# Performance work log

Hardware: AMD Instinct MI355X
Metric: run time of the kernel (lower is better)

The kernel has to match this reference:

```python
import jax, jax.numpy as jnp
import numpy as np

IN_FEATURES = 4096
OUT_FEATURES = 4096
TOKENS = 8192
QMAX = 127.0


def setup_inputs() -> dict:
    key = jax.random.key(0)
    k1, k2, k3, k4 = jax.random.split(key, 4)
    x = jax.random.normal(k1, (TOKENS, IN_FEATURES), dtype=jnp.float32)
    # int8 quantized weights in [-127, 127]
    Wq = jax.random.randint(k2, (OUT_FEATURES, IN_FEATURES), -127, 128, dtype=jnp.int32).astype(jnp.int8)
    # per-row absmax scales (positive)
    row_scales = jax.random.uniform(k3, (OUT_FEATURES,), dtype=jnp.float32, minval=0.01, maxval=1.0)
    bias_param = jax.random.normal(k4, (OUT_FEATURES,), dtype=jnp.float32)
    return {"x": x, "Wq": Wq, "row_scales": row_scales, "bias_param": bias_param}


def reference(x, Wq, row_scales, bias_param):
    # rowwise dequant: W[o, i] = Wq[o, i] * row_scales[o] / 127
    W_dequant = Wq.astype(x.dtype) * (row_scales.astype(x.dtype) / QMAX)[:, None]  # [O, I]
    Y = jnp.matmul(x, W_dequant.T)  # [T, O]
    return Y + bias_param.astype(x.dtype)
```

## Files before the change

### kernel.cpp

```cpp
#include <hip/hip_runtime.h>

#define M_TOK 8192
#define N_OUT 4096
#define K_IN  4096

#define AS1 __attribute__((address_space(1)))
#define AS3 __attribute__((address_space(3)))

typedef __attribute__((ext_vector_type(4))) int i32x4;
typedef __attribute__((ext_vector_type(16))) int i32x16;

template <int OFF>
__device__ __forceinline__ i32x4 dsri(unsigned addr) {
    i32x4 r;
    asm volatile("ds_read_b128 %0, %1 offset:%2" : "=v"(r) : "v"(addr), "n"(OFF));
    return r;
}


__global__ __launch_bounds__(256) void quant_x_kernel(
    const float* __restrict__ x, signed char* __restrict__ xq,
    float* __restrict__ tok_scale)
{
    const int row = blockIdx.x;
    const float4* xr = reinterpret_cast<const float4*>(x + (size_t)row * K_IN);
    const int t = threadIdx.x;
    float4 v[4];
    float m = 0.f;
#pragma unroll
    for (int i = 0; i < 4; ++i) {
        v[i] = xr[t + 256 * i];
        m = fmaxf(m, fmaxf(fmaxf(fabsf(v[i].x), fabsf(v[i].y)),
                           fmaxf(fabsf(v[i].z), fabsf(v[i].w))));
    }
#pragma unroll
    for (int off = 32; off >= 1; off >>= 1)
        m = fmaxf(m, __shfl_xor(m, off, 64));
    __shared__ float wmax[4];
    if ((t & 63) == 0) wmax[t >> 6] = m;
    __syncthreads();
    m = fmaxf(fmaxf(wmax[0], wmax[1]), fmaxf(wmax[2], wmax[3]));
    if (t == 0) tok_scale[row] = m * (1.0f / 127.0f);
    const float inv = (m > 0.f) ? (127.0f / m) : 0.f;
    int* xqi = reinterpret_cast<int*>(xq + (size_t)row * K_IN);
#pragma unroll
    for (int i = 0; i < 4; ++i) {
        const int q0 = __float2int_rn(v[i].x * inv) & 255;
        const int q1 = __float2int_rn(v[i].y * inv) & 255;
        const int q2 = __float2int_rn(v[i].z * inv) & 255;
        const int q3 = __float2int_rn(v[i].w * inv) & 255;
        xqi[t + 256 * i] = q0 | (q1 << 8) | (q2 << 16) | (q3 << 24);
    }
}


__global__ void pack_w_kernel(const int* __restrict__ wq, signed char* __restrict__ o) {
    const int n4 = (N_OUT * K_IN) / 4;
    int* o4 = reinterpret_cast<int*>(o);
    const int stride = gridDim.x * blockDim.x;
    for (int i = blockIdx.x * blockDim.x + threadIdx.x; i < n4; i += stride) {
        const int4 a = reinterpret_cast<const int4*>(wq)[i];
        o4[i] = (a.x & 255) | ((a.y & 255) << 8) | ((a.z & 255) << 16) | ((a.w & 255) << 24);
    }
}


#define BKB 64
#define NKT (K_IN / BKB)
#define SLOT 32768
#define NSLOT 4

#define MFMA(a, b, c) c = __builtin_amdgcn_mfma_i32_32x32x32_i8(a, b, c, 0, 0, 0)

#define RD12(P, aB, bB)                        \
    P##_A0 = dsri<0>(aB);                      \
    P##_A1 = dsri<2048>(aB);                   \
    P##_A2 = dsri<4096>(aB);                   \
    P##_A3 = dsri<6144>(aB);                   \
    P##_B0 = dsri<0>(bB);                      \
    P##_B1 = dsri<2048>(bB);                   \
    P##_A4 = dsri<1024>(aB);                   \
    P##_A5 = dsri<3072>(aB);                   \
    P##_A6 = dsri<5120>(aB);                   \
    P##_A7 = dsri<7168>(aB);                   \
    P##_B2 = dsri<1024>(bB);                   \
    P##_B3 = dsri<3072>(bB);

#define CL8_0(P)                                              \
    MFMA(P##_A0, P##_B0, acc00); MFMA(P##_A0, P##_B1, acc01); \
    MFMA(P##_A1, P##_B0, acc10); MFMA(P##_A1, P##_B1, acc11); \
    MFMA(P##_A2, P##_B0, acc20); MFMA(P##_A2, P##_B1, acc21); \
    MFMA(P##_A3, P##_B0, acc30); MFMA(P##_A3, P##_B1, acc31);

#define CL8_1(P)                                              \
    MFMA(P##_A4, P##_B2, acc00); MFMA(P##_A4, P##_B3, acc01); \
    MFMA(P##_A5, P##_B2, acc10); MFMA(P##_A5, P##_B3, acc11); \
    MFMA(P##_A6, P##_B2, acc20); MFMA(P##_A6, P##_B3, acc21); \
    MFMA(P##_A7, P##_B2, acc30); MFMA(P##_A7, P##_B3, acc31);

#define GBODY(T, C, N, DO_STAGE)                                          \
    {                                                                     \
        asm volatile("s_waitcnt lgkmcnt(6)" ::: "memory");                \
        __builtin_amdgcn_sched_barrier(0);                                \
        __builtin_amdgcn_s_setprio(1);                                    \
        CL8_0(C)                                                          \
        __builtin_amdgcn_s_setprio(0);                                    \
        __builtin_amdgcn_sched_barrier(0);                                \
        const unsigned aN_ = aBase + (unsigned)((((T) + 1) & 3) * SLOT);  \
        const unsigned bN_ = bBase + (unsigned)((((T) + 1) & 3) * SLOT);  \
        RD12(N, aN_, bN_)                                                 \
        if (DO_STAGE) stageAB((T) + 3);                                   \
        asm volatile("s_waitcnt lgkmcnt(12)" ::: "memory");               \
        __builtin_amdgcn_sched_barrier(0);                                \
        __builtin_amdgcn_s_setprio(1);                                    \
        CL8_1(C)                                                          \
        __builtin_amdgcn_s_setprio(0);                                    \
        __builtin_amdgcn_sched_barrier(0);                                \
        if (DO_STAGE) { asm volatile("s_waitcnt vmcnt(4)" ::: "memory"); }\
        else          { asm volatile("s_waitcnt vmcnt(0)" ::: "memory"); }\
        __builtin_amdgcn_sched_barrier(0);                                \
        __builtin_amdgcn_s_barrier();                                     \
        __builtin_amdgcn_sched_barrier(0);                                \
    }

#define GFINAL(C)                                                         \
    {                                                                     \
        asm volatile("s_waitcnt lgkmcnt(6)" ::: "memory");                \
        __builtin_amdgcn_sched_barrier(0);                                \
        __builtin_amdgcn_s_setprio(1);                                    \
        CL8_0(C)                                                          \
        __builtin_amdgcn_s_setprio(0);                                    \
        asm volatile("s_waitcnt lgkmcnt(0)" ::: "memory");                \
        __builtin_amdgcn_sched_barrier(0);                                \
        __builtin_amdgcn_s_setprio(1);                                    \
        CL8_1(C)                                                          \
        __builtin_amdgcn_s_setprio(0);                                    \
        __builtin_amdgcn_sched_barrier(0);                                \
    }

__global__ __launch_bounds__(512, 2) void qgemm_i8p_kernel(
    const signed char* __restrict__ xq,
    const signed char* __restrict__ wq8,
    const float* __restrict__ tok_scale,
    const float* __restrict__ row_scales,
    const float* __restrict__ bias,
    float* __restrict__ out)
{
    __shared__ __align__(16) char smem[NSLOT * SLOT + 1024];

    const int tid = threadIdx.x;
    const int l = tid & 63;
    const int w = tid >> 6;
    const int wr = w >> 2;
    const int wc = w & 3;

    const int bid = blockIdx.x;
    const int swz = (bid & 7) * 64 + (bid >> 3);
    const int bm = swz >> 4;
    const int bn = swz & 15;

    const signed char* aS = xq  + (size_t)(bm * 256 + w * 32 + (l & 31)) * K_IN + (l >> 5) * 16;
    const signed char* bS = wq8 + (size_t)(bn * 256 + w * 32 + (l & 31)) * K_IN + (l >> 5) * 16;
    char* aDst = smem + w * 2048;
    char* bDst = smem + 16384 + w * 2048;

    auto stageAB = [&](int tt) {
        const int sb = (tt & 3) * SLOT;
        const signed char* a0 = aS + tt * BKB;
        const signed char* b0 = bS + tt * BKB;
        __builtin_amdgcn_global_load_lds((const AS1 void*)a0,        (AS3 void*)(aDst + sb),        16, 0, 0);
        __builtin_amdgcn_global_load_lds((const AS1 void*)(a0 + 32), (AS3 void*)(aDst + sb + 1024), 16, 0, 0);
        __builtin_amdgcn_global_load_lds((const AS1 void*)b0,        (AS3 void*)(bDst + sb),        16, 0, 0);
        __builtin_amdgcn_global_load_lds((const AS1 void*)(b0 + 32), (AS3 void*)(bDst + sb + 1024), 16, 0, 0);
    };

    const unsigned sbase = (unsigned)(uintptr_t)(AS3 char*)smem;
    const unsigned aBase = sbase + (unsigned)(wr * 8192 + l * 16);
    const unsigned bBase = sbase + 16384u + (unsigned)(wc * 4096 + l * 16);

    i32x16 acc00 = {0}, acc01 = {0}, acc10 = {0}, acc11 = {0};
    i32x16 acc20 = {0}, acc21 = {0}, acc30 = {0}, acc31 = {0};

    i32x4 X_A0, X_A1, X_A2, X_A3, X_A4, X_A5, X_A6, X_A7, X_B0, X_B1, X_B2, X_B3;
    i32x4 Y_A0, Y_A1, Y_A2, Y_A3, Y_A4, Y_A5, Y_A6, Y_A7, Y_B0, Y_B1, Y_B2, Y_B3;

    stageAB(0); stageAB(1); stageAB(2);
    asm volatile("s_waitcnt vmcnt(4)" ::: "memory");
    __builtin_amdgcn_sched_barrier(0);
    __builtin_amdgcn_s_barrier();
    __builtin_amdgcn_sched_barrier(0);
    RD12(X, aBase, bBase)

    for (int t = 0; t < 62; t += 2) {
        GBODY(t,     X, Y, (t + 3 < NKT));
        GBODY(t + 1, Y, X, (t + 4 < NKT));
    }
    GBODY(62, X, Y, false);
    GFINAL(Y)

    float* ts = (float*)(smem + NSLOT * SLOT);
    if (tid < 256) ts[tid] = tok_scale[bm * 256 + tid];
    __syncthreads();

    const int cl = l & 31;
    const int rg4 = (l >> 5) * 4;
    const int gcol0 = bn * 256 + wc * 64;
    float cs[2], bb[2];
#pragma unroll
    for (int nb = 0; nb < 2; ++nb) {
        const int col = gcol0 + nb * 32 + cl;
        cs[nb] = row_scales[col] * (1.0f / 127.0f);
        bb[nb] = bias[col];
    }
    const i32x16* accs[4][2] = {{&acc00, &acc01}, {&acc10, &acc11},
                                {&acc20, &acc21}, {&acc30, &acc31}};
#pragma unroll
    for (int mb = 0; mb < 4; ++mb) {
#pragma unroll
        for (int reg = 0; reg < 16; ++reg) {
            const int rloc = wr * 128 + mb * 32 + (reg & 3) + 8 * (reg >> 2) + rg4;
            const float tsv = ts[rloc];
            float* orow = out + (size_t)(bm * 256 + rloc) * N_OUT + gcol0 + cl;
#pragma unroll
            for (int nb = 0; nb < 2; ++nb) {
                const int a = (*accs[mb][nb])[reg];
                orow[nb * 32] = (float)a * tsv * cs[nb] + bb[nb];
            }
        }
    }
}


extern "C" void kernel_launch(void* const* d_in, const int* in_sizes, int n_in,
                              void* d_out, int out_size, void* d_ws, size_t ws_size,
                              hipStream_t stream) {
    const float* x = (const float*)d_in[0];
    const int* wq = (const int*)d_in[1];
    const float* row_scales = (const float*)d_in[2];
    const float* bias = (const float*)d_in[3];
    float* out = (float*)d_out;

    signed char* xq8 = (signed char*)d_ws;
    signed char* wq8 = xq8 + (size_t)M_TOK * K_IN;
    float* tok_scale = (float*)(wq8 + (size_t)N_OUT * K_IN);
    (void)ws_size;

    quant_x_kernel<<<M_TOK, 256, 0, stream>>>(x, xq8, tok_scale);
    pack_w_kernel<<<2048, 256, 0, stream>>>(wq, wq8);

    const int nblocks = (M_TOK / 256) * (N_OUT / 256);
    qgemm_i8p_kernel<<<nblocks, 512, 0, stream>>>(
        xq8, wq8, tok_scale, row_scales, bias, out);
}
```

Baseline: 210.5 us.

## Store quantized operands in MFMA fragment-major layout for contiguous GEMM loads

```diff
diff --git a/kernel.cpp b/kernel.cpp
--- a/kernel.cpp
+++ b/kernel.cpp
@@ -17,50 +17,87 @@
     return r;
 }
 
-
-__global__ __launch_bounds__(256) void quant_x_kernel(
-    const float* __restrict__ x, signed char* __restrict__ xq,
+__device__ __forceinline__ int pack4(float a, float b, float c, float d, float inv) {
+    const int q0 = __float2int_rn(a * inv) & 255;
+    const int q1 = __float2int_rn(b * inv) & 255;
+    const int q2 = __float2int_rn(c * inv) & 255;
+    const int q3 = __float2int_rn(d * inv) & 255;
+    return q0 | (q1 << 8) | (q2 << 16) | (q3 << 24);
+}
+
+
+__global__ __launch_bounds__(256) void quant_x_frag_kernel(
+    const float* __restrict__ x, signed char* __restrict__ xqF,
     float* __restrict__ tok_scale)
 {
-    const int row = blockIdx.x;
-    const float4* xr = reinterpret_cast<const float4*>(x + (size_t)row * K_IN);
+    __shared__ float sm_inv[32];
     const int t = threadIdx.x;
-    float4 v[4];
-    float m = 0.f;
-#pragma unroll
-    for (int i = 0; i < 4; ++i) {
-        v[i] = xr[t + 256 * i];
-        m = fmaxf(m, fmaxf(fmaxf(fabsf(v[i].x), fabsf(v[i].y)),
-                           fmaxf(fabsf(v[i].z), fabsf(v[i].w))));
-    }
-#pragma unroll
-    for (int off = 32; off >= 1; off >>= 1)
-        m = fmaxf(m, __shfl_xor(m, off, 64));
-    __shared__ float wmax[4];
-    if ((t & 63) == 0) wmax[t >> 6] = m;
+    const int R0 = blockIdx.x * 32;
+
+    {
+        const int r = R0 + (t >> 3);
+        const float4* xr4 = reinterpret_cast<const float4*>(x) + (size_t)r * 1024;
+        float m = 0.f;
+        for (int p = 0; p < 128; ++p) {
+            const float4 v = xr4[(t & 7) + 8 * p];
+            m = fmaxf(m, fmaxf(fmaxf(fabsf(v.x), fabsf(v.y)),
+                               fmaxf(fabsf(v.z), fabsf(v.w))));
+        }
+        m = fmaxf(m, __shfl_xor(m, 1, 64));
+        m = fmaxf(m, __shfl_xor(m, 2, 64));
+        m = fmaxf(m, __shfl_xor(m, 4, 64));
+        if ((t & 7) == 0) {
+            sm_inv[t >> 3] = (m > 0.f) ? (127.0f / m) : 0.f;
+            tok_scale[r] = m * (1.0f / 127.0f);
+        }
+    }
     __syncthreads();
-    m = fmaxf(fmaxf(wmax[0], wmax[1]), fmaxf(wmax[2], wmax[3]));
-    if (t == 0) tok_scale[row] = m * (1.0f / 127.0f);
-    const float inv = (m > 0.f) ? (127.0f / m) : 0.f;
-    int* xqi = reinterpret_cast<int*>(xq + (size_t)row * K_IN);
-#pragma unroll
-    for (int i = 0; i < 4; ++i) {
-        const int q0 = __float2int_rn(v[i].x * inv) & 255;
-        const int q1 = __float2int_rn(v[i].y * inv) & 255;
-        const int q2 = __float2int_rn(v[i].z * inv) & 255;
-        const int q3 = __float2int_rn(v[i].w * inv) & 255;
-        xqi[t + 256 * i] = q0 | (q1 << 8) | (q2 << 16) | (q3 << 24);
-    }
-}
-
-
-__global__ void pack_w_kernel(const int* __restrict__ wq, signed char* __restrict__ o) {
-    const int n4 = (N_OUT * K_IN) / 4;
-    int* o4 = reinterpret_cast<int*>(o);
-    const int stride = gridDim.x * blockDim.x;
-    for (int i = blockIdx.x * blockDim.x + threadIdx.x; i < n4; i += stride) {
-        const int4 a = reinterpret_cast<const int4*>(wq)[i];
-        o4[i] = (a.x & 255) | ((a.y & 255) << 8) | ((a.z & 255) << 16) | ((a.w & 255) << 24);
+
+    const int l = t & 63;
+    const int W = t >> 6;
+    const int r = R0 + (l & 31);
+    const float inv = sm_inv[l & 31];
+    const float4* xr4 = reinterpret_cast<const float4*>(x) + (size_t)r * 1024;
+    i32x4* outF = reinterpret_cast<i32x4*>(xqF) + (size_t)blockIdx.x * 128 * 64 + l;
+#pragma unroll 4
+    for (int p = 0; p < 32; ++p) {
+        const int f = W + 4 * p;
+        const int c4 = f * 8 + (l >> 5) * 4;
+        const float4 v0 = xr4[c4 + 0];
+        const float4 v1 = xr4[c4 + 1];
+        const float4 v2 = xr4[c4 + 2];
+        const float4 v3 = xr4[c4 + 3];
+        i32x4 o;
+        o[0] = pack4(v0.x, v0.y, v0.z, v0.w, inv);
+        o[1] = pack4(v1.x, v1.y, v1.z, v1.w, inv);
+        o[2] = pack4(v2.x, v2.y, v2.z, v2.w, inv);
+        o[3] = pack4(v3.x, v3.y, v3.z, v3.w, inv);
+        outF[(size_t)f * 64] = o;
+    }
+}
+
+
+__global__ __launch_bounds__(256) void pack_w_frag_kernel(
+    const int* __restrict__ wq, signed char* __restrict__ wqF)
+{
+    const int t = threadIdx.x;
+    const int l = t & 63;
+    const int W = t >> 6;
+    const int R0 = blockIdx.x * 32;
+    const int r = R0 + (l & 31);
+    const int4* wr4 = reinterpret_cast<const int4*>(wq) + (size_t)r * 1024;
+    i32x4* outF = reinterpret_cast<i32x4*>(wqF) + (size_t)blockIdx.x * 128 * 64 + l;
+#pragma unroll 4
+    for (int p = 0; p < 32; ++p) {
+        const int f = W + 4 * p;
+        const int c4 = f * 8 + (l >> 5) * 4;
+        i32x4 o;
+#pragma unroll
+        for (int j = 0; j < 4; ++j) {
+            const int4 a = wr4[c4 + j];
+            o[j] = (a.x & 255) | ((a.y & 255) << 8) | ((a.z & 255) << 16) | ((a.w & 255) << 24);
+        }
+        outF[(size_t)f * 64] = o;
     }
 }
 
@@ -138,9 +175,9 @@
         __builtin_amdgcn_sched_barrier(0);                                \
     }
 
-__global__ __launch_bounds__(512, 2) void qgemm_i8p_kernel(
-    const signed char* __restrict__ xq,
-    const signed char* __restrict__ wq8,
+__global__ __launch_bounds__(512, 2) void qgemm_i8f_kernel(
+    const signed char* __restrict__ xqF,
+    const signed char* __restrict__ wqF,
     const float* __restrict__ tok_scale,
     const float* __restrict__ row_scales,
     const float* __restrict__ bias,
@@ -159,19 +196,19 @@
     const int bm = swz >> 4;
     const int bn = swz & 15;
 
-    const signed char* aS = xq  + (size_t)(bm * 256 + w * 32 + (l & 31)) * K_IN + (l >> 5) * 16;
-    const signed char* bS = wq8 + (size_t)(bn * 256 + w * 32 + (l & 31)) * K_IN + (l >> 5) * 16;
+    const signed char* aS = xqF + ((size_t)(bm * 8 + w) * 128) * 1024 + (size_t)l * 16;
+    const signed char* bS = wqF + ((size_t)(bn * 8 + w) * 128) * 1024 + (size_t)l * 16;
     char* aDst = smem + w * 2048;
     char* bDst = smem + 16384 + w * 2048;
 
     auto stageAB = [&](int tt) {
         const int sb = (tt & 3) * SLOT;
-        const signed char* a0 = aS + tt * BKB;
-        const signed char* b0 = bS + tt * BKB;
-        __builtin_amdgcn_global_load_lds((const AS1 void*)a0,        (AS3 void*)(aDst + sb),        16, 0, 0);
-        __builtin_amdgcn_global_load_lds((const AS1 void*)(a0 + 32), (AS3 void*)(aDst + sb + 1024), 16, 0, 0);
-        __builtin_amdgcn_global_load_lds((const AS1 void*)b0,        (AS3 void*)(bDst + sb),        16, 0, 0);
-        __builtin_amdgcn_global_load_lds((const AS1 void*)(b0 + 32), (AS3 void*)(bDst + sb + 1024), 16, 0, 0);
+        const signed char* a0 = aS + (size_t)tt * 2048;
+        const signed char* b0 = bS + (size_t)tt * 2048;
+        __builtin_amdgcn_global_load_lds((const AS1 void*)a0,          (AS3 void*)(aDst + sb),        16, 0, 0);
+        __builtin_amdgcn_global_load_lds((const AS1 void*)(a0 + 1024), (AS3 void*)(aDst + sb + 1024), 16, 0, 0);
+        __builtin_amdgcn_global_load_lds((const AS1 void*)b0,          (AS3 void*)(bDst + sb),        16, 0, 0);
+        __builtin_amdgcn_global_load_lds((const AS1 void*)(b0 + 1024), (AS3 void*)(bDst + sb + 1024), 16, 0, 0);
     };
 
     const unsigned sbase = (unsigned)(uintptr_t)(AS3 char*)smem;
@@ -240,15 +277,15 @@
     const float* bias = (const float*)d_in[3];
     float* out = (float*)d_out;
 
-    signed char* xq8 = (signed char*)d_ws;
-    signed char* wq8 = xq8 + (size_t)M_TOK * K_IN;
-    float* tok_scale = (float*)(wq8 + (size_t)N_OUT * K_IN);
+    signed char* xqF = (signed char*)d_ws;
+    signed char* wqF = xqF + (size_t)M_TOK * K_IN;
+    float* tok_scale = (float*)(wqF + (size_t)N_OUT * K_IN);
     (void)ws_size;
 
-    quant_x_kernel<<<M_TOK, 256, 0, stream>>>(x, xq8, tok_scale);
-    pack_w_kernel<<<2048, 256, 0, stream>>>(wq, wq8);
+    quant_x_frag_kernel<<<M_TOK / 32, 256, 0, stream>>>(x, xqF, tok_scale);
+    pack_w_frag_kernel<<<N_OUT / 32, 256, 0, stream>>>(wq, wqF);
 
     const int nblocks = (M_TOK / 256) * (N_OUT / 256);
-    qgemm_i8p_kernel<<<nblocks, 512, 0, stream>>>(
-        xq8, wq8, tok_scale, row_scales, bias, out);
-}
+    qgemm_i8f_kernel<<<nblocks, 512, 0, stream>>>(
+        xqF, wqF, tok_scale, row_scales, bias, out);
+}
```

Result: slower. 236.2 us (+12.2%).

## Pre-tile int8 activations and weights into MFMA fragment order for contiguous loads

Applied to the files above, without the earlier changes.

```diff
diff --git a/kernel.cpp b/kernel.cpp
--- a/kernel.cpp
+++ b/kernel.cpp
@@ -54,13 +54,65 @@
 }
 
 
-__global__ void pack_w_kernel(const int* __restrict__ wq, signed char* __restrict__ o) {
-    const int n4 = (N_OUT * K_IN) / 4;
-    int* o4 = reinterpret_cast<int*>(o);
-    const int stride = gridDim.x * blockDim.x;
-    for (int i = blockIdx.x * blockDim.x + threadIdx.x; i < n4; i += stride) {
-        const int4 a = reinterpret_cast<const int4*>(wq)[i];
-        o4[i] = (a.x & 255) | ((a.y & 255) << 8) | ((a.z & 255) << 16) | ((a.w & 255) << 24);
+__global__ __launch_bounds__(256) void retile_x_kernel(
+    const signed char* __restrict__ xq8, signed char* __restrict__ xqF)
+{
+    __shared__ __align__(16) char lds[32768];
+    const int t = threadIdx.x;
+    const int rb = blockIdx.x >> 2;
+    const int kc = blockIdx.x & 3;
+
+    const size_t srcBase = (size_t)rb * 32 * K_IN + (size_t)kc * 1024;
+#pragma unroll
+    for (int j = 0; j < 8; ++j) {
+        const int u = j * 256 + t;
+        const int row = u >> 6, gc = u & 63;
+        const i32x4 v = *reinterpret_cast<const i32x4*>(
+            xq8 + srcBase + (size_t)row * K_IN + gc * 16);
+        *reinterpret_cast<i32x4*>(
+            lds + ((row * 64 + (gc ^ (row & 7))) * 16)) = v;
+    }
+    __syncthreads();
+
+    const int l = t & 63;
+    const int W = t >> 6;
+    const int row = l & 31;
+    const int hi = l >> 5;
+    i32x4* dst0 = reinterpret_cast<i32x4*>(xqF) +
+                  ((size_t)rb * 128 + kc * 32) * 64 + l;
+#pragma unroll
+    for (int i = 0; i < 8; ++i) {
+        const int kfl = W * 8 + i;
+        const int gc = (kfl * 2 + hi) ^ (row & 7);
+        const i32x4 v = *reinterpret_cast<const i32x4*>(
+            lds + ((row * 64 + gc) * 16));
+        dst0[(size_t)kfl * 64] = v;
+    }
+}
+
+
+__global__ __launch_bounds__(256) void pack_w_frag_kernel(
+    const int* __restrict__ wq, signed char* __restrict__ wqF)
+{
+    const int t = threadIdx.x;
+    const int l = t & 63;
+    const int W = t >> 6;
+    const int rb = blockIdx.x >> 3;
+    const int pc = blockIdx.x & 7;
+    const int r = rb * 32 + (l & 31);
+    const int4* wr4 = reinterpret_cast<const int4*>(wq) + (size_t)r * 1024;
+    i32x4* outF = reinterpret_cast<i32x4*>(wqF) + (size_t)rb * 128 * 64 + l;
+#pragma unroll
+    for (int q = 0; q < 4; ++q) {
+        const int f = W + 4 * (pc * 4 + q);
+        const int c4 = f * 8 + (l >> 5) * 4;
+        i32x4 o;
+#pragma unroll
+        for (int j = 0; j < 4; ++j) {
+            const int4 a = wr4[c4 + j];
+            o[j] = (a.x & 255) | ((a.y & 255) << 8) | ((a.z & 255) << 16) | ((a.w & 255) << 24);
+        }
+        outF[(size_t)f * 64] = o;
     }
 }
 
@@ -138,9 +190,9 @@
         __builtin_amdgcn_sched_barrier(0);                                \
     }
 
-__global__ __launch_bounds__(512, 2) void qgemm_i8p_kernel(
-    const signed char* __restrict__ xq,
-    const signed char* __restrict__ wq8,
+__global__ __launch_bounds__(512, 2) void qgemm_i8f_kernel(
+    const signed char* __restrict__ xqF,
+    const signed char* __restrict__ wqF,
     const float* __restrict__ tok_scale,
     const float* __restrict__ row_scales,
     const float* __restrict__ bias,
@@ -159,19 +211,19 @@
     const int bm = swz >> 4;
     const int bn = swz & 15;
 
-    const signed char* aS = xq  + (size_t)(bm * 256 + w * 32 + (l & 31)) * K_IN + (l >> 5) * 16;
-    const signed char* bS = wq8 + (size_t)(bn * 256 + w * 32 + (l & 31)) * K_IN + (l >> 5) * 16;
+    const signed char* aS = xqF + ((size_t)(bm * 8 + w) * 128) * 1024 + (size_t)l * 16;
+    const signed char* bS = wqF + ((size_t)(bn * 8 + w) * 128) * 1024 + (size_t)l * 16;
     char* aDst = smem + w * 2048;
     char* bDst = smem + 16384 + w * 2048;
 
     auto stageAB = [&](int tt) {
         const int sb = (tt & 3) * SLOT;
-        const signed char* a0 = aS + tt * BKB;
-        const signed char* b0 = bS + tt * BKB;
-        __builtin_amdgcn_global_load_lds((const AS1 void*)a0,        (AS3 void*)(aDst + sb),        16, 0, 0);
-        __builtin_amdgcn_global_load_lds((const AS1 void*)(a0 + 32), (AS3 void*)(aDst + sb + 1024), 16, 0, 0);
-        __builtin_amdgcn_global_load_lds((const AS1 void*)b0,        (AS3 void*)(bDst + sb),        16, 0, 0);
-        __builtin_amdgcn_global_load_lds((const AS1 void*)(b0 + 32), (AS3 void*)(bDst + sb + 1024), 16, 0, 0);
+        const signed char* a0 = aS + (size_t)tt * 2048;
+        const signed char* b0 = bS + (size_t)tt * 2048;
+        __builtin_amdgcn_global_load_lds((const AS1 void*)a0,          (AS3 void*)(aDst + sb),        16, 0, 0);
+        __builtin_amdgcn_global_load_lds((const AS1 void*)(a0 + 1024), (AS3 void*)(aDst + sb + 1024), 16, 0, 0);
+        __builtin_amdgcn_global_load_lds((const AS1 void*)b0,          (AS3 void*)(bDst + sb),        16, 0, 0);
+        __builtin_amdgcn_global_load_lds((const AS1 void*)(b0 + 1024), (AS3 void*)(bDst + sb + 1024), 16, 0, 0);
     };
 
     const unsigned sbase = (unsigned)(uintptr_t)(AS3 char*)smem;
@@ -241,14 +293,16 @@
     float* out = (float*)d_out;
 
     signed char* xq8 = (signed char*)d_ws;
-    signed char* wq8 = xq8 + (size_t)M_TOK * K_IN;
-    float* tok_scale = (float*)(wq8 + (size_t)N_OUT * K_IN);
+    signed char* xqF = xq8 + (size_t)M_TOK * K_IN;
+    signed char* wqF = xqF + (size_t)M_TOK * K_IN;
+    float* tok_scale = (float*)(wqF + (size_t)N_OUT * K_IN);
     (void)ws_size;
 
     quant_x_kernel<<<M_TOK, 256, 0, stream>>>(x, xq8, tok_scale);
-    pack_w_kernel<<<2048, 256, 0, stream>>>(wq, wq8);
+    pack_w_frag_kernel<<<1024, 256, 0, stream>>>(wq, wqF);
+    retile_x_kernel<<<1024, 256, 0, stream>>>(xq8, xqF);
 
     const int nblocks = (M_TOK / 256) * (N_OUT / 256);
-    qgemm_i8p_kernel<<<nblocks, 512, 0, stream>>>(
-        xq8, wq8, tok_scale, row_scales, bias, out);
-}
+    qgemm_i8f_kernel<<<nblocks, 512, 0, stream>>>(
+        xqF, wqF, tok_scale, row_scales, bias, out);
+}
```

After: 192.1 us. -8.7%, faster.
